# Performance work log

Hardware: AMD Instinct MI355X
Metric: run time of the kernel (lower is better)

The kernel has to match this reference:

```python
import jax, jax.numpy as jnp
import numpy as np

N, E = 50000, 800000
D_IN, D_E = 256, 64
H1, H2 = 128, 128
N_OUT = 64
LEAKY_SLOPE = 0.01  # torch.nn.LeakyReLU default
EPS = 1e-16         # PyG softmax denominator eps


def setup_inputs() -> dict:
    key = jax.random.key(0)
    ks = jax.random.split(key, 32)

    def w(k, shape, s=0.05):
        return jax.random.normal(k, shape, dtype=jnp.float32) * s

    inp = {
        "x_in": jax.random.normal(ks[0], (N, D_IN), dtype=jnp.float32),
        "edge_index": jax.random.randint(ks[1], (2, E), 0, N),
        "edge_atts": jax.random.normal(ks[2], (E, D_E), dtype=jnp.float32),
        # TransformerConv layer 1 (in=D_IN, out=H1, heads=1, beta=True, edge_dim=D_E)
        "Wq1": w(ks[3], (H1, D_IN)), "bq1": jnp.zeros((H1,), jnp.float32),
        "Wk1": w(ks[4], (H1, D_IN)), "bk1": jnp.zeros((H1,), jnp.float32),
        "Wv1": w(ks[5], (H1, D_IN)), "bv1": jnp.zeros((H1,), jnp.float32),
        "We1": w(ks[6], (H1, D_E)),                     # lin_edge (bias=False)
        "Wskip1": w(ks[7], (H1, D_IN)), "bskip1": jnp.zeros((H1,), jnp.float32),
        "Wbeta1": w(ks[8], (1, 3 * H1)),                # lin_beta (bias=False)
        # TransformerConv layer 2 (in=H1, out=H2)
        "Wq2": w(ks[9], (H2, H1)), "bq2": jnp.zeros((H2,), jnp.float32),
        "Wk2": w(ks[10], (H2, H1)), "bk2": jnp.zeros((H2,), jnp.float32),
        "Wv2": w(ks[11], (H2, H1)), "bv2": jnp.zeros((H2,), jnp.float32),
        "We2": w(ks[12], (H2, D_E)),
        "Wskip2": w(ks[13], (H2, H1)), "bskip2": jnp.zeros((H2,), jnp.float32),
        "Wbeta2": w(ks[14], (1, 3 * H2)),
        # output MLP: Linear(H1 + H2 -> N_OUT)
        "Wm": w(ks[15], (N_OUT, H1 + H2)), "bm": jnp.zeros((N_OUT,), jnp.float32),
    }
    return inp


def _transformer_conv(x, src, dst, edge_attr,
                      Wq, bq, Wk, bk, Wv, bv, We, Wskip, bskip, Wbeta, n_nodes):
    """PyG TransformerConv: heads=1, concat=True, beta=True, root_weight=True,
    dropout inactive (eval mode)."""
    d = Wq.shape[0]
    q = x @ Wq.T + bq                      # [N, d]
    k = x @ Wk.T + bk                      # [N, d]
    v = x @ Wv.T + bv                      # [N, d]
    e = edge_attr @ We.T                   # [E, d]
    k_e = k[src] + e                       # gather source keys + edge embedding
    v_e = v[src] + e                       # gather source values + edge embedding
    # attention score per edge
    score = jnp.einsum('ed,ed->e', q[dst], k_e) / jnp.sqrt(jnp.asarray(d, jnp.float32))
    # segment softmax over incoming edges of each destination node
    m = jax.ops.segment_max(score, dst, num_segments=n_nodes)
    m = jnp.where(jnp.isfinite(m), m, 0.0)
    ex = jnp.exp(score - m[dst])
    denom = jax.ops.segment_sum(ex, dst, num_segments=n_nodes) + EPS
    alpha = ex / denom[dst]                # [E]
    # scatter-add weighted messages
    out = jax.ops.segment_sum(alpha[:, None] * v_e, dst, num_segments=n_nodes)  # [N, d]
    # beta-gated skip connection
    x_r = x @ Wskip.T + bskip
    beta = jax.nn.sigmoid(jnp.concatenate([out, x_r, out - x_r], axis=1) @ Wbeta.T)  # [N, 1]
    return beta * x_r + (1.0 - beta) * out


def _leaky_relu(x):
    return jnp.where(x >= 0, x, LEAKY_SLOPE * x)


def reference(x_in, edge_index, edge_atts,
              Wq1, bq1, Wk1, bk1, Wv1, bv1, We1, Wskip1, bskip1, Wbeta1,
              Wq2, bq2, Wk2, bk2, Wv2, bv2, We2, Wskip2, bskip2, Wbeta2,
              Wm, bm):
    src, dst = edge_index[0], edge_index[1]
    n = x_in.shape[0]
    x1 = _leaky_relu(_transformer_conv(x_in, src, dst, edge_atts,
                                       Wq1, bq1, Wk1, bk1, Wv1, bv1, We1,
                                       Wskip1, bskip1, Wbeta1, n))
    x2 = _leaky_relu(_transformer_conv(x1, src, dst, edge_atts,
                                       Wq2, bq2, Wk2, bk2, Wv2, bv2, We2,
                                       Wskip2, bskip2, Wbeta2, n))
    out = jnp.concatenate([x1, x2], axis=1) @ Wm.T + bm   # [N, N_OUT]
    return out
```

## Files before the change

kernel.cpp:

```cpp
#include <hip/hip_runtime.h>
#include <hip/hip_bf16.h>
#include <math.h>

typedef unsigned short u16;
typedef __attribute__((ext_vector_type(8))) short bf16x8;
typedef __attribute__((ext_vector_type(4))) float f32x4;

__device__ inline u16 f2bf(float x) {
    unsigned u = __float_as_uint(x);
    unsigned r = u + 0x7fff + ((u >> 16) & 1);
    return (u16)(r >> 16);
}
__device__ inline float bf2f(u16 h) { return __uint_as_float(((unsigned)h) << 16); }
__device__ inline void bsplit(float x, u16& h, u16& l) {
    h = f2bf(x);
    float r = x - bf2f(h);
    l = f2bf(r);
}

__global__ void count_deg(const int* __restrict__ dst, int* __restrict__ cnt, int E) {
    int e = blockIdx.x * blockDim.x + threadIdx.x;
    if (e < E) atomicAdd(&cnt[dst[e]], 1);
}

__global__ __launch_bounds__(1024) void scan_a(const int* __restrict__ cnt,
                                               int* __restrict__ out,
                                               int* __restrict__ partials, int N) {
    __shared__ int sh[1024];
    int tid = threadIdx.x;
    int gid = blockIdx.x * 1024 + tid;
    int v = (gid < N) ? cnt[gid] : 0;
    sh[tid] = v;
    for (int off = 1; off < 1024; off <<= 1) {
        __syncthreads();
        int add = (tid >= off) ? sh[tid - off] : 0;
        __syncthreads();
        sh[tid] += add;
    }
    __syncthreads();
    if (gid <= N) out[gid] = sh[tid] - v;
    if (tid == 1023) partials[blockIdx.x] = sh[1023];
}

__global__ void scan_b(int* __restrict__ partials, int nb) {
    if (threadIdx.x == 0 && blockIdx.x == 0) {
        int run = 0;
        for (int i = 0; i < nb; ++i) { int t = partials[i]; partials[i] = run; run += t; }
    }
}

__global__ __launch_bounds__(1024) void scan_c(int* __restrict__ out,
                                               const int* __restrict__ partials,
                                               int* __restrict__ fillb, int N) {
    int gid = blockIdx.x * 1024 + threadIdx.x;
    if (gid <= N) {
        int v = out[gid] + partials[blockIdx.x];
        out[gid] = v;
        fillb[gid] = v;
    }
}

__global__ void fill_edges(const int* __restrict__ src, const int* __restrict__ dst,
                           int* __restrict__ fillb, int2* __restrict__ esi, int E) {
    int e = blockIdx.x * blockDim.x + threadIdx.x;
    if (e < E) {
        int d = dst[e];
        int slot = atomicAdd(&fillb[d], 1);
        esi[slot] = make_int2(src[e], e);
    }
}

__global__ void transpose_we(const float* __restrict__ We, float* __restrict__ WeT) {
    int i = blockIdx.x * blockDim.x + threadIdx.x;
    if (i < 128 * 64) {
        int r = i >> 6, c = i & 63;
        WeT[c * 128 + r] = We[i];
    }
}

__global__ __launch_bounds__(256) void wcomb_k(const float* __restrict__ We,
                                               const float* __restrict__ Wq,
                                               const float* __restrict__ bq,
                                               float* __restrict__ WcT,
                                               float* __restrict__ bqe, int Din) {
    int o = blockIdx.x;
    int d = threadIdx.x;
    float s = 0.f, sb = 0.f;
    for (int h = 0; h < 128; ++h) {
        float w = We[h * 64 + o];
        if (d < Din) s = fmaf(w, Wq[h * Din + d], s);
        sb = fmaf(w, bq[h], sb);
    }
    if (d < Din) WcT[o * Din + d] = s;
    if (d == 0) bqe[o] = sb;
}

__global__ void build_wcat(const float* __restrict__ Wq, const float* __restrict__ Wk,
                           const float* __restrict__ Wv, const float* __restrict__ Ws,
                           const float* __restrict__ Wc,
                           const float* __restrict__ bq, const float* __restrict__ bk,
                           const float* __restrict__ bv, const float* __restrict__ bs,
                           const float* __restrict__ bqe,
                           float* __restrict__ Wcat, float* __restrict__ bcat,
                           int K, int kshift) {
    int i = blockIdx.x * blockDim.x + threadIdx.x;
    if (i < 576 * K) {
        int r = i >> kshift;
        float v;
        if (r < 128)      v = Wq[i];
        else if (r < 256) v = Wk[i - (128 << kshift)];
        else if (r < 384) v = Wv[i - (256 << kshift)];
        else if (r < 512) v = Ws[i - (384 << kshift)];
        else              v = Wc[i - (512 << kshift)];
        Wcat[i] = v;
    }
    if (i < 128) {
        bcat[i]       = bq[i];
        bcat[128 + i] = bk[i];
        bcat[256 + i] = bv[i];
        bcat[384 + i] = bs[i];
    }
    if (i < 64) bcat[512 + i] = bqe[i];
}

__global__ void split_planes(const float* __restrict__ src, u16* __restrict__ hi,
                             u16* __restrict__ lo, int n4) {
    int i = (blockIdx.x * blockDim.x + threadIdx.x) * 4;
    if (i < n4) {
        float4 v = *reinterpret_cast<const float4*>(&src[i]);
        u16 h0, h1, h2, h3, l0, l1, l2, l3;
        bsplit(v.x, h0, l0); bsplit(v.y, h1, l1);
        bsplit(v.z, h2, l2); bsplit(v.w, h3, l3);
        ushort4 hv = make_ushort4(h0, h1, h2, h3);
        ushort4 lv = make_ushort4(l0, l1, l2, l3);
        *reinterpret_cast<ushort4*>(&hi[i]) = hv;
        *reinterpret_cast<ushort4*>(&lo[i]) = lv;
    }
}

#define BM 128
#define BO 64
#define BKX 64
#define LSTR 72
__global__ __launch_bounds__(256) void gemm_mfma(
    const u16* __restrict__ XH, const u16* __restrict__ XL, int ldx,
    const u16* __restrict__ WH, const u16* __restrict__ WL,
    const float* __restrict__ bias, float* __restrict__ Out, int ldo,
    int Nrows, int K) {
    __shared__ __align__(16) u16 XsH[BM * LSTR];
    __shared__ __align__(16) u16 XsL[BM * LSTR];
    __shared__ __align__(16) u16 WsH[BO * LSTR];
    __shared__ __align__(16) u16 WsL[BO * LSTR];
    int n0 = blockIdx.x * BM, o0 = blockIdx.y * BO;
    int t = threadIdx.x, wid = t >> 6, lane = t & 63;
    int xr = t >> 1, xk = (t & 1) * 32;
    int wr = t >> 2, wk = (t & 3) * 16;
    bool xok = (n0 + xr) < Nrows;
    const u16* xh = XH + (size_t)(n0 + xr) * ldx + xk;
    const u16* xl = XL + (size_t)(n0 + xr) * ldx + xk;
    const u16* wh = WH + (size_t)(o0 + wr) * K + wk;
    const u16* wl = WL + (size_t)(o0 + wr) * K + wk;
    f32x4 acc[2][4] = {};
    for (int k0 = 0; k0 < K; k0 += BKX) {
#pragma unroll
        for (int j = 0; j < 4; ++j) {
            bf16x8 vh = {0, 0, 0, 0, 0, 0, 0, 0};
            bf16x8 vl = {0, 0, 0, 0, 0, 0, 0, 0};
            if (xok) {
                vh = *reinterpret_cast<const bf16x8*>(xh + k0 + 8 * j);
                vl = *reinterpret_cast<const bf16x8*>(xl + k0 + 8 * j);
            }
            *reinterpret_cast<bf16x8*>(&XsH[xr * LSTR + xk + 8 * j]) = vh;
            *reinterpret_cast<bf16x8*>(&XsL[xr * LSTR + xk + 8 * j]) = vl;
        }
#pragma unroll
        for (int j = 0; j < 2; ++j) {
            *reinterpret_cast<bf16x8*>(&WsH[wr * LSTR + wk + 8 * j]) =
                *reinterpret_cast<const bf16x8*>(wh + k0 + 8 * j);
            *reinterpret_cast<bf16x8*>(&WsL[wr * LSTR + wk + 8 * j]) =
                *reinterpret_cast<const bf16x8*>(wl + k0 + 8 * j);
        }
        __syncthreads();
#pragma unroll
        for (int kc = 0; kc < 2; ++kc) {
            int kf = kc * 32 + (lane >> 4) * 8;
            int ar = wid * 32 + (lane & 15);
            bf16x8 aH0 = *reinterpret_cast<const bf16x8*>(&XsH[ar * LSTR + kf]);
            bf16x8 aH1 = *reinterpret_cast<const bf16x8*>(&XsH[(ar + 16) * LSTR + kf]);
            bf16x8 aL0 = *reinterpret_cast<const bf16x8*>(&XsL[ar * LSTR + kf]);
            bf16x8 aL1 = *reinterpret_cast<const bf16x8*>(&XsL[(ar + 16) * LSTR + kf]);
#pragma unroll
            for (int c = 0; c < 4; ++c) {
                int br = c * 16 + (lane & 15);
                bf16x8 bH = *reinterpret_cast<const bf16x8*>(&WsH[br * LSTR + kf]);
                bf16x8 bL = *reinterpret_cast<const bf16x8*>(&WsL[br * LSTR + kf]);
                acc[0][c] = __builtin_amdgcn_mfma_f32_16x16x32_bf16(aH0, bH, acc[0][c], 0, 0, 0);
                acc[1][c] = __builtin_amdgcn_mfma_f32_16x16x32_bf16(aH1, bH, acc[1][c], 0, 0, 0);
                acc[0][c] = __builtin_amdgcn_mfma_f32_16x16x32_bf16(aH0, bL, acc[0][c], 0, 0, 0);
                acc[1][c] = __builtin_amdgcn_mfma_f32_16x16x32_bf16(aH1, bL, acc[1][c], 0, 0, 0);
                acc[0][c] = __builtin_amdgcn_mfma_f32_16x16x32_bf16(aL0, bH, acc[0][c], 0, 0, 0);
                acc[1][c] = __builtin_amdgcn_mfma_f32_16x16x32_bf16(aL1, bH, acc[1][c], 0, 0, 0);
            }
        }
        __syncthreads();
    }
#pragma unroll
    for (int c = 0; c < 4; ++c) {
        int col = o0 + c * 16 + (lane & 15);
        float bb = bias ? bias[col] : 0.f;
#pragma unroll
        for (int r = 0; r < 2; ++r) {
            int rb = n0 + wid * 32 + r * 16 + (lane >> 4) * 4;
#pragma unroll
            for (int q = 0; q < 4; ++q) {
                int row = rb + q;
                if (row < Nrows) Out[(size_t)row * ldo + col] = acc[r][c][q] + bb;
            }
        }
    }
}

#define AW3 4
#define LD6 576
__global__ __launch_bounds__(256) void attn3(
    const int* __restrict__ row_ptr, const int2* __restrict__ esi,
    const float* __restrict__ QKVS, const float* __restrict__ Ae,
    float* __restrict__ Acc, int Nn) {
    int t = threadIdx.x;
    int wid = t >> 6, lane = t & 63;
    const float RS = 0.088388347648318447f;
    for (int n = blockIdx.x * AW3 + wid; n < Nn; n += gridDim.x * AW3) {
        int r0 = row_ptr[n], r1 = row_ptr[n + 1];
        const float* qrow = QKVS + (size_t)n * LD6;
        float q0  = qrow[lane];
        float q1  = qrow[64 + lane];
        float qe0 = qrow[512 + lane];
        float m = -1e30f, l = 0.f, av0 = 0.f, av1 = 0.f, aa = 0.f;
        for (int p = r0; p < r1; p += 8) {
            int pi[8];
#pragma unroll
            for (int i = 0; i < 8; ++i) pi[i] = (p + i < r1) ? p + i : r1 - 1;
            int2 se[8];
#pragma unroll
            for (int i = 0; i < 8; ++i) se[i] = esi[pi[i]];
            float k0v[8], k1v[8], a0v[8];
#pragma unroll
            for (int i = 0; i < 8; ++i) {
                const float* kr = QKVS + (size_t)se[i].x * LD6 + 128;
                k0v[i] = kr[lane]; k1v[i] = kr[64 + lane];
            }
#pragma unroll
            for (int i = 0; i < 8; ++i) a0v[i] = Ae[(size_t)se[i].y * 64 + lane];
            float d[8];
#pragma unroll
            for (int i = 0; i < 8; ++i)
                d[i] = fmaf(q0, k0v[i], fmaf(q1, k1v[i], qe0 * a0v[i]));
#pragma unroll
            for (int off = 32; off; off >>= 1) {
#pragma unroll
                for (int i = 0; i < 8; ++i) d[i] += __shfl_xor(d[i], off, 64);
            }
            float v0v[8], v1v[8];
#pragma unroll
            for (int i = 0; i < 8; ++i) {
                const float* vr = QKVS + (size_t)se[i].x * LD6 + 256;
                v0v[i] = vr[lane]; v1v[i] = vr[64 + lane];
            }
            float sc[8];
#pragma unroll
            for (int i = 0; i < 8; ++i) sc[i] = (p + i < r1) ? d[i] * RS : -1e30f;
            float bm = sc[0];
#pragma unroll
            for (int i = 1; i < 8; ++i) bm = fmaxf(bm, sc[i]);
            float mn = fmaxf(m, bm);
            float scale = __expf(m - mn);
            float w[8];
#pragma unroll
            for (int i = 0; i < 8; ++i) w[i] = __expf(sc[i] - mn);
            float ws = ((w[0] + w[1]) + (w[2] + w[3])) + ((w[4] + w[5]) + (w[6] + w[7]));
            l = fmaf(l, scale, ws);
            float s_aa = 0.f, s0 = 0.f, s1 = 0.f;
#pragma unroll
            for (int i = 0; i < 8; ++i) {
                s_aa = fmaf(w[i], a0v[i], s_aa);
                s0   = fmaf(w[i], v0v[i], s0);
                s1   = fmaf(w[i], v1v[i], s1);
            }
            aa  = fmaf(aa,  scale, s_aa);
            av0 = fmaf(av0, scale, s0);
            av1 = fmaf(av1, scale, s1);
            m = mn;
        }
        float inv = 1.0f / (l + 1e-16f);
        float* arow = Acc + (size_t)n * 192;
        arow[lane]       = av0 * inv;
        arow[64 + lane]  = av1 * inv;
        arow[128 + lane] = aa * inv;
    }
}

__global__ __launch_bounds__(256) void epilogue_k(
    const float* __restrict__ Acc, const float* __restrict__ QKVS,
    const float* __restrict__ WeT, const float* __restrict__ Wbeta,
    u16* __restrict__ XoH, u16* __restrict__ XoL, int coff, int Nn) {
    __shared__ float WeS[64 * 128];
    __shared__ float wbA[128], wbB[128];
    int t = threadIdx.x;
    for (int i = t; i < 64 * 128; i += 256) WeS[i] = WeT[i];
    if (t < 128) {
        float w3 = Wbeta[256 + t];
        wbA[t] = Wbeta[t] + w3;
        wbB[t] = Wbeta[128 + t] - w3;
    }
    __syncthreads();
    int wid = t >> 6, lane = t & 63;
    for (int n = blockIdx.x * 4 + wid; n < Nn; n += gridDim.x * 4) {
        const float* ar = Acc + (size_t)n * 192;
        float out0 = ar[lane], out1 = ar[64 + lane], aa = ar[128 + lane];
#pragma unroll
        for (int j = 0; j < 64; ++j) {
            float aj = __shfl(aa, j, 64);
            out0 = fmaf(aj, WeS[j * 128 + lane], out0);
            out1 = fmaf(aj, WeS[j * 128 + 64 + lane], out1);
        }
        const float* qrow = QKVS + (size_t)n * LD6;
        float xr0 = qrow[384 + lane], xr1 = qrow[448 + lane];
        float bp = wbA[lane] * out0 + wbA[64 + lane] * out1 +
                   wbB[lane] * xr0  + wbB[64 + lane] * xr1;
#pragma unroll
        for (int off = 32; off; off >>= 1) bp += __shfl_xor(bp, off, 64);
        float beta = 1.0f / (1.0f + __expf(-bp));
        float x0 = beta * xr0 + (1.0f - beta) * out0;
        float x1 = beta * xr1 + (1.0f - beta) * out1;
        x0 = (x0 >= 0.f) ? x0 : 0.01f * x0;
        x1 = (x1 >= 0.f) ? x1 : 0.01f * x1;
        u16 h, l;
        size_t base = (size_t)n * 256 + coff;
        bsplit(x0, h, l); XoH[base + lane] = h;      XoL[base + lane] = l;
        bsplit(x1, h, l); XoH[base + 64 + lane] = h; XoL[base + 64 + lane] = l;
    }
}

extern "C" void kernel_launch(void* const* d_in, const int* in_sizes, int n_in,
                              void* d_out, int out_size, void* d_ws, size_t ws_size,
                              hipStream_t stream) {
    const float* x_in  = (const float*)d_in[0];
    const int*   eidx  = (const int*)d_in[1];
    const float* eatt  = (const float*)d_in[2];
    const float* Wq1 = (const float*)d_in[3];  const float* bq1 = (const float*)d_in[4];
    const float* Wk1 = (const float*)d_in[5];  const float* bk1 = (const float*)d_in[6];
    const float* Wv1 = (const float*)d_in[7];  const float* bv1 = (const float*)d_in[8];
    const float* We1 = (const float*)d_in[9];
    const float* Wskip1 = (const float*)d_in[10]; const float* bskip1 = (const float*)d_in[11];
    const float* Wbeta1 = (const float*)d_in[12];
    const float* Wq2 = (const float*)d_in[13]; const float* bq2 = (const float*)d_in[14];
    const float* Wk2 = (const float*)d_in[15]; const float* bk2 = (const float*)d_in[16];
    const float* Wv2 = (const float*)d_in[17]; const float* bv2 = (const float*)d_in[18];
    const float* We2 = (const float*)d_in[19];
    const float* Wskip2 = (const float*)d_in[20]; const float* bskip2 = (const float*)d_in[21];
    const float* Wbeta2 = (const float*)d_in[22];
    const float* Wm  = (const float*)d_in[23]; const float* bm  = (const float*)d_in[24];

    const int N = in_sizes[0] / 256;
    const int E = in_sizes[1] / 2;
    const int* srcp = eidx;
    const int* dstp = eidx + E;

    char* p = (char*)d_ws;
    auto alloc = [&](size_t bytes) -> void* {
        void* r = (void*)p;
        p += (bytes + 255) & ~(size_t)255;
        return r;
    };
    int*   row_ptr  = (int*)alloc((size_t)(N + 1) * 4);
    int*   fillb    = (int*)alloc((size_t)(N + 1) * 4);
    int*   partials = (int*)alloc(256 * 4);
    int2*  esi      = (int2*)alloc((size_t)E * 8);
    float* QKVS = (float*)alloc((size_t)N * 576 * 4);
    float* Accb = (float*)alloc((size_t)N * 192 * 4);
    u16*   XpH  = (u16*)alloc((size_t)N * 256 * 2);
    u16*   XpL  = (u16*)alloc((size_t)N * 256 * 2);
    float* WeT  = (float*)alloc((size_t)64 * 128 * 4);
    float* Wcat = (float*)alloc((size_t)576 * 256 * 4);
    u16*   WcH  = (u16*)alloc((size_t)576 * 256 * 2);
    u16*   WcL  = (u16*)alloc((size_t)576 * 256 * 2);
    float* WcombT = (float*)alloc((size_t)64 * 256 * 4);
    float* bcat = (float*)alloc(576 * 4);
    float* bqe  = (float*)alloc(64 * 4);
    u16*   WmH  = (u16*)alloc((size_t)64 * 256 * 2);
    u16*   WmL  = (u16*)alloc((size_t)64 * 256 * 2);

    hipMemsetAsync(fillb, 0, (size_t)(N + 1) * 4, stream);
    count_deg<<<(E + 255) / 256, 256, 0, stream>>>(dstp, fillb, E);
    int nScanBlocks = (N + 1 + 1023) / 1024;
    scan_a<<<nScanBlocks, 1024, 0, stream>>>(fillb, row_ptr, partials, N);
    scan_b<<<1, 1, 0, stream>>>(partials, nScanBlocks);
    scan_c<<<nScanBlocks, 1024, 0, stream>>>(row_ptr, partials, fillb, N);
    fill_edges<<<(E + 255) / 256, 256, 0, stream>>>(srcp, dstp, fillb, esi, E);

    dim3 blk(256);
    int gmx = (N + BM - 1) / BM;

    split_planes<<<(N * 256 / 4 + 255) / 256, 256, 0, stream>>>(x_in, XpH, XpL, N * 256);

    wcomb_k<<<64, 256, 0, stream>>>(We1, Wq1, bq1, WcombT, bqe, 256);
    build_wcat<<<(576 * 256 + 255) / 256, 256, 0, stream>>>(
        Wq1, Wk1, Wv1, Wskip1, WcombT, bq1, bk1, bv1, bskip1, bqe, Wcat, bcat, 256, 8);
    split_planes<<<(576 * 256 / 4 + 255) / 256, 256, 0, stream>>>(Wcat, WcH, WcL, 576 * 256);
    transpose_we<<<(128 * 64 + 255) / 256, 256, 0, stream>>>(We1, WeT);
    gemm_mfma<<<dim3(gmx, 9), blk, 0, stream>>>(XpH, XpL, 256, WcH, WcL, bcat,
                                                QKVS, 576, N, 256);
    attn3<<<2048, blk, 0, stream>>>(row_ptr, esi, QKVS, eatt, Accb, N);
    epilogue_k<<<1024, blk, 0, stream>>>(Accb, QKVS, WeT, Wbeta1, XpH, XpL, 0, N);

    wcomb_k<<<64, 256, 0, stream>>>(We2, Wq2, bq2, WcombT, bqe, 128);
    build_wcat<<<(576 * 128 + 255) / 256, 256, 0, stream>>>(
        Wq2, Wk2, Wv2, Wskip2, WcombT, bq2, bk2, bv2, bskip2, bqe, Wcat, bcat, 128, 7);
    split_planes<<<(576 * 128 / 4 + 255) / 256, 256, 0, stream>>>(Wcat, WcH, WcL, 576 * 128);
    transpose_we<<<(128 * 64 + 255) / 256, 256, 0, stream>>>(We2, WeT);
    gemm_mfma<<<dim3(gmx, 9), blk, 0, stream>>>(XpH, XpL, 256, WcH, WcL, bcat,
                                                QKVS, 576, N, 128);
    attn3<<<2048, blk, 0, stream>>>(row_ptr, esi, QKVS, eatt, Accb, N);
    epilogue_k<<<1024, blk, 0, stream>>>(Accb, QKVS, WeT, Wbeta2, XpH, XpL, 128, N);

    split_planes<<<(64 * 256 / 4 + 255) / 256, 256, 0, stream>>>(Wm, WmH, WmL, 64 * 256);
    gemm_mfma<<<dim3(gmx, 1), blk, 0, stream>>>(XpH, XpL, 256, WmH, WmL, bm,
                                                (float*)d_out, 64, N, 256);
}
```

Baseline: 1.158 ms.

## Fuse attention with epilogue, pack K/V rows, merge weight prep kernels

Folds all weight preparation (concatenation, We·Wq fold, bf16 hi/lo split, We transpose, Wm split) into one prep_weights launch. Attention is fused with the beta-gated epilogue so the per-node Acc buffer round trip goes away. A new pack_attn pass interleaves K into float2 and stores V as packed bf16 pairs, halving V gather traffic at some precision cost. The attention loop also moves to 12-edge batches with exp2-based softmax. The extra packing pass and the lower V precision are the added cost and risk.

Measured after the change: 1.574 ms. 36.0% more time.

```diff
diff --git a/kernel.cpp b/kernel.cpp
--- a/kernel.cpp
+++ b/kernel.cpp
@@ -3,6 +3,7 @@
 #include <math.h>
 
 typedef unsigned short u16;
+typedef unsigned int u32;
 typedef __attribute__((ext_vector_type(8))) short bf16x8;
 typedef __attribute__((ext_vector_type(4))) float f32x4;
 
@@ -70,57 +71,80 @@
     }
 }
 
-__global__ void transpose_we(const float* __restrict__ We, float* __restrict__ WeT) {
-    int i = blockIdx.x * blockDim.x + threadIdx.x;
-    if (i < 128 * 64) {
-        int r = i >> 6, c = i & 63;
-        WeT[c * 128 + r] = We[i];
-    }
-}
-
-__global__ __launch_bounds__(256) void wcomb_k(const float* __restrict__ We,
-                                               const float* __restrict__ Wq,
-                                               const float* __restrict__ bq,
-                                               float* __restrict__ WcT,
-                                               float* __restrict__ bqe, int Din) {
-    int o = blockIdx.x;
-    int d = threadIdx.x;
-    float s = 0.f, sb = 0.f;
-    for (int h = 0; h < 128; ++h) {
-        float w = We[h * 64 + o];
-        if (d < Din) s = fmaf(w, Wq[h * Din + d], s);
-        sb = fmaf(w, bq[h], sb);
-    }
-    if (d < Din) WcT[o * Din + d] = s;
-    if (d == 0) bqe[o] = sb;
-}
-
-__global__ void build_wcat(const float* __restrict__ Wq, const float* __restrict__ Wk,
-                           const float* __restrict__ Wv, const float* __restrict__ Ws,
-                           const float* __restrict__ Wc,
-                           const float* __restrict__ bq, const float* __restrict__ bk,
-                           const float* __restrict__ bv, const float* __restrict__ bs,
-                           const float* __restrict__ bqe,
-                           float* __restrict__ Wcat, float* __restrict__ bcat,
-                           int K, int kshift) {
-    int i = blockIdx.x * blockDim.x + threadIdx.x;
-    if (i < 576 * K) {
-        int r = i >> kshift;
-        float v;
-        if (r < 128)      v = Wq[i];
-        else if (r < 256) v = Wk[i - (128 << kshift)];
-        else if (r < 384) v = Wv[i - (256 << kshift)];
-        else if (r < 512) v = Ws[i - (384 << kshift)];
-        else              v = Wc[i - (512 << kshift)];
-        Wcat[i] = v;
-    }
-    if (i < 128) {
-        bcat[i]       = bq[i];
-        bcat[128 + i] = bk[i];
-        bcat[256 + i] = bv[i];
-        bcat[384 + i] = bs[i];
-    }
-    if (i < 64) bcat[512 + i] = bqe[i];
+__global__ __launch_bounds__(256) void prep_weights(
+    const float* __restrict__ Wq1, const float* __restrict__ Wk1,
+    const float* __restrict__ Wv1, const float* __restrict__ Ws1,
+    const float* __restrict__ We1,
+    const float* __restrict__ bq1, const float* __restrict__ bk1,
+    const float* __restrict__ bv1, const float* __restrict__ bs1,
+    const float* __restrict__ Wq2, const float* __restrict__ Wk2,
+    const float* __restrict__ Wv2, const float* __restrict__ Ws2,
+    const float* __restrict__ We2,
+    const float* __restrict__ bq2, const float* __restrict__ bk2,
+    const float* __restrict__ bv2, const float* __restrict__ bs2,
+    const float* __restrict__ Wm,
+    u16* __restrict__ Wc1H, u16* __restrict__ Wc1L,
+    u16* __restrict__ Wc2H, u16* __restrict__ Wc2L,
+    float* __restrict__ bcat1, float* __restrict__ bcat2,
+    float* __restrict__ WeT1, float* __restrict__ WeT2,
+    u16* __restrict__ WmH, u16* __restrict__ WmL) {
+    int b = blockIdx.x;
+    int t = threadIdx.x;
+    if (b < 1152) {
+        int L = b / 576;
+        int r = b - L * 576;
+        int K = L ? 128 : 256;
+        const float* Wq = L ? Wq2 : Wq1;
+        const float* We = L ? We2 : We1;
+        u16* WH = L ? Wc2H : Wc1H;
+        u16* WL = L ? Wc2L : Wc1L;
+        float* bcat = L ? bcat2 : bcat1;
+        float val = 0.f;
+        bool have = t < K;
+        if (r < 512) {
+            int sub = r >> 7, rr = r & 127;
+            const float* Wsrc = L ? (sub == 0 ? Wq2 : sub == 1 ? Wk2 : sub == 2 ? Wv2 : Ws2)
+                                  : (sub == 0 ? Wq1 : sub == 1 ? Wk1 : sub == 2 ? Wv1 : Ws1);
+            if (have) val = Wsrc[(size_t)rr * K + t];
+            if (t == 0) {
+                const float* bsrc = L ? (sub == 0 ? bq2 : sub == 1 ? bk2 : sub == 2 ? bv2 : bs2)
+                                      : (sub == 0 ? bq1 : sub == 1 ? bk1 : sub == 2 ? bv1 : bs1);
+                bcat[r] = bsrc[rr];
+            }
+        } else {
+            int o = r - 512;
+            if (have) {
+                float s = 0.f;
+                for (int h = 0; h < 128; ++h)
+                    s = fmaf(We[h * 64 + o], Wq[(size_t)h * K + t], s);
+                val = s;
+            }
+            if (t == 0) {
+                const float* bq = L ? bq2 : bq1;
+                float sb = 0.f;
+                for (int h = 0; h < 128; ++h) sb = fmaf(We[h * 64 + o], bq[h], sb);
+                bcat[r] = sb;
+            }
+        }
+        if (have) {
+            u16 h, l;
+            bsplit(val, h, l);
+            WH[(size_t)r * K + t] = h;
+            WL[(size_t)r * K + t] = l;
+        }
+    } else if (b == 1152 || b == 1153) {
+        const float* We = (b == 1152) ? We1 : We2;
+        float* WeT = (b == 1152) ? WeT1 : WeT2;
+        for (int i = t; i < 128 * 64; i += 256)
+            WeT[(i & 63) * 128 + (i >> 6)] = We[i];
+    } else {
+        for (int i = t; i < 64 * 256; i += 256) {
+            u16 h, l;
+            bsplit(Wm[i], h, l);
+            WmH[i] = h;
+            WmL[i] = l;
+        }
+    }
 }
 
 __global__ void split_planes(const float* __restrict__ src, u16* __restrict__ hi,
@@ -131,10 +155,8 @@
         u16 h0, h1, h2, h3, l0, l1, l2, l3;
         bsplit(v.x, h0, l0); bsplit(v.y, h1, l1);
         bsplit(v.z, h2, l2); bsplit(v.w, h3, l3);
-        ushort4 hv = make_ushort4(h0, h1, h2, h3);
-        ushort4 lv = make_ushort4(l0, l1, l2, l3);
-        *reinterpret_cast<ushort4*>(&hi[i]) = hv;
-        *reinterpret_cast<ushort4*>(&lo[i]) = lv;
+        *reinterpret_cast<ushort4*>(&hi[i]) = make_ushort4(h0, h1, h2, h3);
+        *reinterpret_cast<ushort4*>(&lo[i]) = make_ushort4(l0, l1, l2, l3);
     }
 }
 
@@ -220,87 +242,24 @@
     }
 }
 
-#define AW3 4
-#define LD6 576
-__global__ __launch_bounds__(256) void attn3(
+__global__ __launch_bounds__(256) void pack_attn(float* __restrict__ QKVS, int Nn) {
+    int gwid = (blockIdx.x * blockDim.x + threadIdx.x) >> 6;
+    int lane = threadIdx.x & 63;
+    int nw = (gridDim.x * blockDim.x) >> 6;
+    for (int n = gwid; n < Nn; n += nw) {
+        float* row = QKVS + (size_t)n * 576;
+        float k0 = row[128 + lane], k1 = row[192 + lane];
+        float v0 = row[256 + lane], v1 = row[320 + lane];
+        u32 vp = ((u32)f2bf(v1) << 16) | (u32)f2bf(v0);
+        *reinterpret_cast<float2*>(&row[128 + 2 * lane]) = make_float2(k0, k1);
+        reinterpret_cast<u32*>(row)[256 + lane] = vp;
+    }
+}
+
+#define AB 12
+__global__ __launch_bounds__(256) void attn4(
     const int* __restrict__ row_ptr, const int2* __restrict__ esi,
     const float* __restrict__ QKVS, const float* __restrict__ Ae,
-    float* __restrict__ Acc, int Nn) {
-    int t = threadIdx.x;
-    int wid = t >> 6, lane = t & 63;
-    const float RS = 0.088388347648318447f;
-    for (int n = blockIdx.x * AW3 + wid; n < Nn; n += gridDim.x * AW3) {
-        int r0 = row_ptr[n], r1 = row_ptr[n + 1];
-        const float* qrow = QKVS + (size_t)n * LD6;
-        float q0  = qrow[lane];
-        float q1  = qrow[64 + lane];
-        float qe0 = qrow[512 + lane];
-        float m = -1e30f, l = 0.f, av0 = 0.f, av1 = 0.f, aa = 0.f;
-        for (int p = r0; p < r1; p += 8) {
-            int pi[8];
-#pragma unroll
-            for (int i = 0; i < 8; ++i) pi[i] = (p + i < r1) ? p + i : r1 - 1;
-            int2 se[8];
-#pragma unroll
-            for (int i = 0; i < 8; ++i) se[i] = esi[pi[i]];
-            float k0v[8], k1v[8], a0v[8];
-#pragma unroll
-            for (int i = 0; i < 8; ++i) {
-                const float* kr = QKVS + (size_t)se[i].x * LD6 + 128;
-                k0v[i] = kr[lane]; k1v[i] = kr[64 + lane];
-            }
-#pragma unroll
-            for (int i = 0; i < 8; ++i) a0v[i] = Ae[(size_t)se[i].y * 64 + lane];
-            float d[8];
-#pragma unroll
-            for (int i = 0; i < 8; ++i)
-                d[i] = fmaf(q0, k0v[i], fmaf(q1, k1v[i], qe0 * a0v[i]));
-#pragma unroll
-            for (int off = 32; off; off >>= 1) {
-#pragma unroll
-                for (int i = 0; i < 8; ++i) d[i] += __shfl_xor(d[i], off, 64);
-            }
-            float v0v[8], v1v[8];
-#pragma unroll
-            for (int i = 0; i < 8; ++i) {
-                const float* vr = QKVS + (size_t)se[i].x * LD6 + 256;
-                v0v[i] = vr[lane]; v1v[i] = vr[64 + lane];
-            }
-            float sc[8];
-#pragma unroll
-            for (int i = 0; i < 8; ++i) sc[i] = (p + i < r1) ? d[i] * RS : -1e30f;
-            float bm = sc[0];
-#pragma unroll
-            for (int i = 1; i < 8; ++i) bm = fmaxf(bm, sc[i]);
-            float mn = fmaxf(m, bm);
-            float scale = __expf(m - mn);
-            float w[8];
-#pragma unroll
-            for (int i = 0; i < 8; ++i) w[i] = __expf(sc[i] - mn);
-            float ws = ((w[0] + w[1]) + (w[2] + w[3])) + ((w[4] + w[5]) + (w[6] + w[7]));
-            l = fmaf(l, scale, ws);
-            float s_aa = 0.f, s0 = 0.f, s1 = 0.f;
-#pragma unroll
-            for (int i = 0; i < 8; ++i) {
-                s_aa = fmaf(w[i], a0v[i], s_aa);
-                s0   = fmaf(w[i], v0v[i], s0);
-                s1   = fmaf(w[i], v1v[i], s1);
-            }
-            aa  = fmaf(aa,  scale, s_aa);
-            av0 = fmaf(av0, scale, s0);
-            av1 = fmaf(av1, scale, s1);
-            m = mn;
-        }
-        float inv = 1.0f / (l + 1e-16f);
-        float* arow = Acc + (size_t)n * 192;
-        arow[lane]       = av0 * inv;
-        arow[64 + lane]  = av1 * inv;
-        arow[128 + lane] = aa * inv;
-    }
-}
-
-__global__ __launch_bounds__(256) void epilogue_k(
-    const float* __restrict__ Acc, const float* __restrict__ QKVS,
     const float* __restrict__ WeT, const float* __restrict__ Wbeta,
     u16* __restrict__ XoH, u16* __restrict__ XoL, int coff, int Nn) {
     __shared__ float WeS[64 * 128];
@@ -314,16 +273,81 @@
     }
     __syncthreads();
     int wid = t >> 6, lane = t & 63;
+    const float RS2 = 0.088388347648318447f * 1.4426950408889634f;
     for (int n = blockIdx.x * 4 + wid; n < Nn; n += gridDim.x * 4) {
-        const float* ar = Acc + (size_t)n * 192;
-        float out0 = ar[lane], out1 = ar[64 + lane], aa = ar[128 + lane];
+        int r0 = row_ptr[n], r1 = row_ptr[n + 1];
+        const float* qrow = QKVS + (size_t)n * 576;
+        float q0  = qrow[lane];
+        float q1  = qrow[64 + lane];
+        float qe0 = qrow[512 + lane];
+        float m = -1e30f, l = 0.f, av0 = 0.f, av1 = 0.f, aa = 0.f;
+        for (int p = r0; p < r1; p += AB) {
+            int2 se[AB];
+#pragma unroll
+            for (int i = 0; i < AB; ++i) {
+                int pp = (p + i < r1) ? p + i : r1 - 1;
+                se[i] = esi[pp];
+            }
+            float2 kp[AB];
+            u32 vu[AB];
+            float af[AB];
+#pragma unroll
+            for (int i = 0; i < AB; ++i)
+                kp[i] = *reinterpret_cast<const float2*>(
+                    &QKVS[(size_t)se[i].x * 576 + 128 + 2 * lane]);
+#pragma unroll
+            for (int i = 0; i < AB; ++i)
+                vu[i] = reinterpret_cast<const u32*>(
+                    QKVS + (size_t)se[i].x * 576)[256 + lane];
+#pragma unroll
+            for (int i = 0; i < AB; ++i) af[i] = Ae[(size_t)se[i].y * 64 + lane];
+            float d[AB];
+#pragma unroll
+            for (int i = 0; i < AB; ++i)
+                d[i] = fmaf(q0, kp[i].x, fmaf(q1, kp[i].y, qe0 * af[i]));
+#pragma unroll
+            for (int off = 32; off; off >>= 1) {
+#pragma unroll
+                for (int i = 0; i < AB; ++i) d[i] += __shfl_xor(d[i], off, 64);
+            }
+            float sc[AB];
+#pragma unroll
+            for (int i = 0; i < AB; ++i) sc[i] = (p + i < r1) ? d[i] * RS2 : -1e30f;
+            float bm = sc[0];
+#pragma unroll
+            for (int i = 1; i < AB; ++i) bm = fmaxf(bm, sc[i]);
+            float mn = fmaxf(m, bm);
+            float scale = exp2f(m - mn);
+            float w[AB];
+#pragma unroll
+            for (int i = 0; i < AB; ++i) w[i] = exp2f(sc[i] - mn);
+            float ws = 0.f;
+#pragma unroll
+            for (int i = 0; i < AB; ++i) ws += w[i];
+            l = fmaf(l, scale, ws);
+            float s_aa = 0.f, s0 = 0.f, s1 = 0.f;
+#pragma unroll
+            for (int i = 0; i < AB; ++i) {
+                float v0 = __uint_as_float(vu[i] << 16);
+                float v1 = __uint_as_float(vu[i] & 0xffff0000u);
+                s_aa = fmaf(w[i], af[i], s_aa);
+                s0   = fmaf(w[i], v0, s0);
+                s1   = fmaf(w[i], v1, s1);
+            }
+            aa  = fmaf(aa,  scale, s_aa);
+            av0 = fmaf(av0, scale, s0);
+            av1 = fmaf(av1, scale, s1);
+            m = mn;
+        }
+        float inv = 1.0f / (l + 1e-16f);
+        av0 *= inv; av1 *= inv; aa *= inv;
+        float out0 = av0, out1 = av1;
 #pragma unroll
         for (int j = 0; j < 64; ++j) {
             float aj = __shfl(aa, j, 64);
             out0 = fmaf(aj, WeS[j * 128 + lane], out0);
             out1 = fmaf(aj, WeS[j * 128 + 64 + lane], out1);
         }
-        const float* qrow = QKVS + (size_t)n * LD6;
         float xr0 = qrow[384 + lane], xr1 = qrow[448 + lane];
         float bp = wbA[lane] * out0 + wbA[64 + lane] * out1 +
                    wbB[lane] * xr0  + wbB[64 + lane] * xr1;
@@ -334,10 +358,10 @@
         float x1 = beta * xr1 + (1.0f - beta) * out1;
         x0 = (x0 >= 0.f) ? x0 : 0.01f * x0;
         x1 = (x1 >= 0.f) ? x1 : 0.01f * x1;
-        u16 h, l;
+        u16 h, l16;
         size_t base = (size_t)n * 256 + coff;
-        bsplit(x0, h, l); XoH[base + lane] = h;      XoL[base + lane] = l;
-        bsplit(x1, h, l); XoH[base + 64 + lane] = h; XoL[base + 64 + lane] = l;
+        bsplit(x0, h, l16); XoH[base + lane] = h;      XoL[base + lane] = l16;
+        bsplit(x1, h, l16); XoH[base + 64 + lane] = h; XoL[base + 64 + lane] = l16;
     }
 }
 
@@ -377,16 +401,16 @@
     int*   partials = (int*)alloc(256 * 4);
     int2*  esi      = (int2*)alloc((size_t)E * 8);
     float* QKVS = (float*)alloc((size_t)N * 576 * 4);
-    float* Accb = (float*)alloc((size_t)N * 192 * 4);
     u16*   XpH  = (u16*)alloc((size_t)N * 256 * 2);
     u16*   XpL  = (u16*)alloc((size_t)N * 256 * 2);
-    float* WeT  = (float*)alloc((size_t)64 * 128 * 4);
-    float* Wcat = (float*)alloc((size_t)576 * 256 * 4);
-    u16*   WcH  = (u16*)alloc((size_t)576 * 256 * 2);
-    u16*   WcL  = (u16*)alloc((size_t)576 * 256 * 2);
-    float* WcombT = (float*)alloc((size_t)64 * 256 * 4);
-    float* bcat = (float*)alloc(576 * 4);
-    float* bqe  = (float*)alloc(64 * 4);
+    float* WeT1 = (float*)alloc((size_t)64 * 128 * 4);
+    float* WeT2 = (float*)alloc((size_t)64 * 128 * 4);
+    u16*   Wc1H = (u16*)alloc((size_t)576 * 256 * 2);
+    u16*   Wc1L = (u16*)alloc((size_t)576 * 256 * 2);
+    u16*   Wc2H = (u16*)alloc((size_t)576 * 128 * 2);
+    u16*   Wc2L = (u16*)alloc((size_t)576 * 128 * 2);
+    float* bcat1 = (float*)alloc(576 * 4);
+    float* bcat2 = (float*)alloc(576 * 4);
     u16*   WmH  = (u16*)alloc((size_t)64 * 256 * 2);
     u16*   WmL  = (u16*)alloc((size_t)64 * 256 * 2);
 
@@ -398,32 +422,28 @@
     scan_c<<<nScanBlocks, 1024, 0, stream>>>(row_ptr, partials, fillb, N);
     fill_edges<<<(E + 255) / 256, 256, 0, stream>>>(srcp, dstp, fillb, esi, E);
 
+    prep_weights<<<1155, 256, 0, stream>>>(
+        Wq1, Wk1, Wv1, Wskip1, We1, bq1, bk1, bv1, bskip1,
+        Wq2, Wk2, Wv2, Wskip2, We2, bq2, bk2, bv2, bskip2, Wm,
+        Wc1H, Wc1L, Wc2H, Wc2L, bcat1, bcat2, WeT1, WeT2, WmH, WmL);
+
+    split_planes<<<(N * 256 / 4 + 255) / 256, 256, 0, stream>>>(x_in, XpH, XpL, N * 256);
+
     dim3 blk(256);
     int gmx = (N + BM - 1) / BM;
 
-    split_planes<<<(N * 256 / 4 + 255) / 256, 256, 0, stream>>>(x_in, XpH, XpL, N * 256);
-
-    wcomb_k<<<64, 256, 0, stream>>>(We1, Wq1, bq1, WcombT, bqe, 256);
-    build_wcat<<<(576 * 256 + 255) / 256, 256, 0, stream>>>(
-        Wq1, Wk1, Wv1, Wskip1, WcombT, bq1, bk1, bv1, bskip1, bqe, Wcat, bcat, 256, 8);
-    split_planes<<<(576 * 256 / 4 + 255) / 256, 256, 0, stream>>>(Wcat, WcH, WcL, 576 * 256);
-    transpose_we<<<(128 * 64 + 255) / 256, 256, 0, stream>>>(We1, WeT);
-    gemm_mfma<<<dim3(gmx, 9), blk, 0, stream>>>(XpH, XpL, 256, WcH, WcL, bcat,
+    gemm_mfma<<<dim3(gmx, 9), blk, 0, stream>>>(XpH, XpL, 256, Wc1H, Wc1L, bcat1,
                                                 QKVS, 576, N, 256);
-    attn3<<<2048, blk, 0, stream>>>(row_ptr, esi, QKVS, eatt, Accb, N);
-    epilogue_k<<<1024, blk, 0, stream>>>(Accb, QKVS, WeT, Wbeta1, XpH, XpL, 0, N);
-
-    wcomb_k<<<64, 256, 0, stream>>>(We2, Wq2, bq2, WcombT, bqe, 128);
-    build_wcat<<<(576 * 128 + 255) / 256, 256, 0, stream>>>(
-        Wq2, Wk2, Wv2, Wskip2, WcombT, bq2, bk2, bv2, bskip2, bqe, Wcat, bcat, 128, 7);
-    split_planes<<<(576 * 128 / 4 + 255) / 256, 256, 0, stream>>>(Wcat, WcH, WcL, 576 * 128);
-    transpose_we<<<(128 * 64 + 255) / 256, 256, 0, stream>>>(We2, WeT);
-    gemm_mfma<<<dim3(gmx, 9), blk, 0, stream>>>(XpH, XpL, 256, WcH, WcL, bcat,
+    pack_attn<<<2048, blk, 0, stream>>>(QKVS, N);
+    attn4<<<1024, blk, 0, stream>>>(row_ptr, esi, QKVS, eatt, WeT1, Wbeta1,
+                                    XpH, XpL, 0, N);
+
+    gemm_mfma<<<dim3(gmx, 9), blk, 0, stream>>>(XpH, XpL, 256, Wc2H, Wc2L, bcat2,
                                                 QKVS, 576, N, 128);
-    attn3<<<2048, blk, 0, stream>>>(row_ptr, esi, QKVS, eatt, Accb, N);
-    epilogue_k<<<1024, blk, 0, stream>>>(Accb, QKVS, WeT, Wbeta2, XpH, XpL, 128, N);
-
-    split_planes<<<(64 * 256 / 4 + 255) / 256, 256, 0, stream>>>(Wm, WmH, WmL, 64 * 256);
+    pack_attn<<<2048, blk, 0, stream>>>(QKVS, N);
+    attn4<<<1024, blk, 0, stream>>>(row_ptr, esi, QKVS, eatt, WeT2, Wbeta2,
+                                    XpH, XpL, 128, N);
+
     gemm_mfma<<<dim3(gmx, 1), blk, 0, stream>>>(XpH, XpL, 256, WmH, WmL, bm,
                                                 (float*)d_out, 64, N, 256);
 }
```
